# Kernel tuning notes

Measured on AMD Instinct MI355X. Metric: run time of the kernel, lower is better.

Reference implementation:

```python
import jax, jax.numpy as jnp
import numpy as np
import math

# ---- static configuration (matches init_kwargs) ----
METADATA = [64, 48, 32]   # channels per l = 0,1,2
MAX_L = 3                 # order_out
N_BATCH = 32768
fact = math.factorial

def _cg_complex(l1, m1, l2, m2, l3, m3):
    # Clebsch-Gordan coefficient <l1 m1 l2 m2 | l3 m3> via Racah formula
    if m1 + m2 != m3 or l3 < abs(l1 - l2) or l3 > l1 + l2:
        return 0.0
    pre = math.sqrt((2*l3+1) * fact(l1+l2-l3) * fact(l1-l2+l3) * fact(-l1+l2+l3) / fact(l1+l2+l3+1))
    pre *= math.sqrt(fact(l1+m1)*fact(l1-m1)*fact(l2+m2)*fact(l2-m2)*fact(l3+m3)*fact(l3-m3))
    kmin = max(0, l2-l3-m1, l1-l3+m2)
    kmax = min(l1+l2-l3, l1-m1, l2+m2)
    s = 0.0
    for k in range(kmin, kmax+1):
        s += (-1)**k / (fact(k)*fact(l1+l2-l3-k)*fact(l1-m1-k)*fact(l2+m2-k)*fact(l3-l2+m1+k)*fact(l3-l1-m2+k))
    return pre * s

def _U(l):
    # complex->real spherical harmonic change of basis, rows = real m', cols = complex m
    U = np.zeros((2*l+1, 2*l+1), dtype=np.complex128)
    for m in range(-l, l+1):
        r = m + l
        if m > 0:
            U[r, m+l] = (-1)**m / math.sqrt(2.0); U[r, -m+l] = 1.0/math.sqrt(2.0)
        elif m == 0:
            U[r, l] = 1.0
        else:
            U[r, m+l] = 1j/math.sqrt(2.0); U[r, -m+l] = -1j*(-1)**m/math.sqrt(2.0)
    return U

def _real_cg(l1, l2, l3):
    Cc = np.zeros((2*l1+1, 2*l2+1, 2*l3+1))
    for m1 in range(-l1, l1+1):
        for m2 in range(-l2, l2+1):
            for m3 in range(-l3, l3+1):
                Cc[m1+l1, m2+l2, m3+l3] = _cg_complex(l1, m1, l2, m2, l3, m3)
    T = np.einsum('am,bn,co,mno->abc', _U(l1), _U(l2), _U(l3).conj(), Cc.astype(np.complex128))
    T = T.imag if np.abs(T.imag).max() > np.abs(T.real).max() else T.real
    return np.ascontiguousarray(T).astype(np.float32)

# ---- static index structures ----
L_IN = len(METADATA)
OFF_IN = np.concatenate([[0], np.cumsum([METADATA[l]*(2*l+1) for l in range(L_IN)])]).astype(np.int64)
DIM_IN = int(OFF_IN[-1])  # 368
PATHS = []
for l1 in range(L_IN):
    for l2 in range(L_IN):
        for l3 in range(abs(l1-l2), min(l1+l2, MAX_L)+1):
            PATHS.append((l1, l2, l3, min(METADATA[l1], METADATA[l2])))
MD_OV = [0]*(MAX_L+1)
for (_, _, l3, ch) in PATHS:
    MD_OV[l3] = max(MD_OV[l3], ch)
OFF_OUT = np.concatenate([[0], np.cumsum([MD_OV[l]*(2*l+1) for l in range(MAX_L+1)])]).astype(np.int64)
DIM_OUT = int(OFF_OUT[-1])  # 672
CG = {(l1, l2, l3): jnp.asarray(_real_cg(l1, l2, l3)) for (l1, l2, l3, _) in PATHS}

_mix_id, _scat = [], []
_base = 0
for (l1, l2, l3, ch) in PATHS:
    for i in range(ch):
        for m in range(2*l3+1):
            _mix_id.append(_base + i)
            _scat.append(int(OFF_OUT[l3]) + i*(2*l3+1) + m)
    _base += ch
MIX_ID = jnp.asarray(np.array(_mix_id, dtype=np.int64))
SCATTER = jnp.asarray(np.array(_scat, dtype=np.int64))
N_MIX = _base  # 688

_chan_in = []
_cb = 0
for l in range(L_IN):
    for i in range(METADATA[l]):
        _chan_in += [_cb + i]*(2*l+1)
    _cb += METADATA[l]
CHAN_IN = jnp.asarray(np.array(_chan_in, dtype=np.int64))
N_KEEP = _cb  # 144
_kin, _kout = [], []
for l in range(L_IN):
    cp = min(METADATA[l], MD_OV[l])
    for i in range(cp):
        for m in range(2*l+1):
            _kin.append(int(OFF_IN[l]) + i*(2*l+1) + m)
            _kout.append(int(OFF_OUT[l]) + i*(2*l+1) + m)
KEEP_IN = jnp.asarray(np.array(_kin, dtype=np.int64))
KEEP_OUT = jnp.asarray(np.array(_kout, dtype=np.int64))

SQ3 = math.sqrt(3.0)

def setup_inputs() -> dict:
    key = jax.random.key(0)
    k1, k2, k3 = jax.random.split(key, 3)
    x = jax.random.normal(k1, (N_BATCH, DIM_IN), dtype=jnp.float32)
    keep_coeff = jax.random.uniform(k2, (N_KEEP,), minval=-SQ3, maxval=SQ3, dtype=jnp.float32)
    mix_coeff = jax.random.uniform(k3, (N_MIX,), minval=-SQ3, maxval=SQ3, dtype=jnp.float32)
    return {"x": x, "keep_coeff": keep_coeff, "mix_coeff": mix_coeff}

def reference(x, keep_coeff, mix_coeff):
    n = x.shape[0]
    # keep path: per-channel coeff broadcast over m components
    x_keep = x * keep_coeff[CHAN_IN]  # [N, 368]
    # CG tensor-product self-coupling (diagonal channel pairing per path)
    tps = []
    for (l1, l2, l3, ch) in PATHS:
        x1 = x[:, OFF_IN[l1]:OFF_IN[l1]+ch*(2*l1+1)].reshape(n, ch, 2*l1+1)
        x2 = x[:, OFF_IN[l2]:OFF_IN[l2]+ch*(2*l2+1)].reshape(n, ch, 2*l2+1)
        tps.append(jnp.einsum('nia,nib,abm->nim', x1, x2, CG[(l1, l2, l3)]).reshape(n, -1))
    cat = jnp.concatenate(tps, axis=1)  # [N, 2576] non-overlapped TP output
    cat = cat * 0.5 * mix_coeff[MIX_ID]
    # scatter (index_add) into overlapped output layout
    out = jnp.zeros((n, DIM_OUT), dtype=x.dtype).at[:, SCATTER].add(cat)
    # gather + add of keep path (index_select + add_)
    out = out.at[:, KEEP_OUT].add(x_keep[:, KEEP_IN])
    return out
```

## Files before the change

### kernel.cpp

```cpp
#include <hip/hip_runtime.h>


namespace cgc {

struct cplx { double re, im; };
constexpr cplx cmul(cplx a, cplx b){ return {a.re*b.re - a.im*b.im, a.re*b.im + a.im*b.re}; }

constexpr double cfact(int n){ double r = 1.0; for (int i = 2; i <= n; ++i) r *= i; return r; }
constexpr double cabsd(double x){ return x < 0 ? -x : x; }

constexpr double csqrtd(double x){
  if (x <= 0.0) return 0.0;
  double g = x > 1.0 ? x : 1.0;
  for (int i = 0; i < 48; ++i) g = 0.5*(g + x/g);
  return g;
}

constexpr double SQRT2 = csqrtd(2.0);

constexpr double cg_complex(int l1,int m1,int l2,int m2,int l3,int m3){
  if (m1 + m2 != m3) return 0.0;
  int lo = l1 > l2 ? l1 - l2 : l2 - l1;
  if (l3 < lo || l3 > l1 + l2) return 0.0;
  double pre = csqrtd((2*l3+1) * cfact(l1+l2-l3)*cfact(l1-l2+l3)*cfact(-l1+l2+l3)/cfact(l1+l2+l3+1));
  pre *= csqrtd(cfact(l1+m1)*cfact(l1-m1)*cfact(l2+m2)*cfact(l2-m2)*cfact(l3+m3)*cfact(l3-m3));
  int kmin = 0;
  if (l2-l3-m1 > kmin) kmin = l2-l3-m1;
  if (l1-l3+m2 > kmin) kmin = l1-l3+m2;
  int kmax = l1+l2-l3;
  if (l1-m1 < kmax) kmax = l1-m1;
  if (l2+m2 < kmax) kmax = l2+m2;
  double s = 0.0;
  for (int k = kmin; k <= kmax; ++k){
    double d = cfact(k)*cfact(l1+l2-l3-k)*cfact(l1-m1-k)*cfact(l2+m2-k)
             * cfact(l3-l2+m1+k)*cfact(l3-l1-m2+k);
    s += ((k & 1) ? -1.0 : 1.0) / d;
  }
  return pre * s;
}

constexpr cplx Uent(int l, int r, int c){
  int m = r - l;
  if (m > 0){
    if (c ==  m + l) return { ((m & 1) ? -1.0 : 1.0)/SQRT2, 0.0 };
    if (c == -m + l) return { 1.0/SQRT2, 0.0 };
    return {0.0, 0.0};
  } else if (m == 0){
    if (c == l) return {1.0, 0.0};
    return {0.0, 0.0};
  } else {
    int ma = -m;
    if (c ==  m + l) return { 0.0, 1.0/SQRT2 };
    if (c == -m + l) return { 0.0, -(((ma & 1) ? -1.0 : 1.0))/SQRT2 };
    return {0.0, 0.0};
  }
}

template<int L1,int L2,int L3>
struct CGData { float w[(2*L1+1)*(2*L2+1)*(2*L3+1)]; };

template<int L1,int L2,int L3>
constexpr CGData<L1,L2,L3> make_cg(){
  constexpr int D1 = 2*L1+1, D2 = 2*L2+1, D3 = 2*L3+1;
  cplx U1[D1*D1] = {}; cplx U2[D2*D2] = {}; cplx U3c[D3*D3] = {};
  for (int r = 0; r < D1; ++r) for (int c = 0; c < D1; ++c) U1[r*D1+c] = Uent(L1, r, c);
  for (int r = 0; r < D2; ++r) for (int c = 0; c < D2; ++c) U2[r*D2+c] = Uent(L2, r, c);
  for (int r = 0; r < D3; ++r) for (int c = 0; c < D3; ++c){
    cplx u = Uent(L3, r, c); u.im = -u.im; U3c[r*D3+c] = u;
  }
  double Cc[D1*D2*D3] = {};
  for (int m1 = -L1; m1 <= L1; ++m1)
    for (int m2 = -L2; m2 <= L2; ++m2){
      int m3 = m1 + m2;
      if (m3 < -L3 || m3 > L3) continue;
      Cc[((m1+L1)*D2 + (m2+L2))*D3 + (m3+L3)] = cg_complex(L1,m1,L2,m2,L3,m3);
    }
  double re[D1*D2*D3] = {}; double im[D1*D2*D3] = {};
  for (int a = 0; a < D1; ++a)
    for (int b = 0; b < D2; ++b)
      for (int c = 0; c < D3; ++c){
        double sre = 0.0, sim = 0.0;
        for (int m = 0; m < D1; ++m)
          for (int n = 0; n < D2; ++n){
            int o = m + n - L1 - L2 + L3;
            if (o < 0 || o >= D3) continue;
            double cc = Cc[(m*D2+n)*D3 + o];
            if (cc == 0.0) continue;
            cplx p = cmul(cmul(U1[a*D1+m], U2[b*D2+n]), U3c[c*D3+o]);
            sre += p.re * cc; sim += p.im * cc;
          }
        re[(a*D2+b)*D3+c] = sre; im[(a*D2+b)*D3+c] = sim;
      }
  double mre = 0.0, mim = 0.0;
  for (int k = 0; k < D1*D2*D3; ++k){
    if (cabsd(re[k]) > mre) mre = cabsd(re[k]);
    if (cabsd(im[k]) > mim) mim = cabsd(im[k]);
  }
  CGData<L1,L2,L3> outv{};
  for (int k = 0; k < D1*D2*D3; ++k){
    double v = (mim > mre) ? im[k] : re[k];
    outv.w[k] = (cabsd(v) < 1e-10) ? 0.0f : (float)v;
  }
  return outv;
}

}

template<int L1,int L2,int L3>
__device__ __forceinline__ void tp_path(const float* xa, const float* xb, float cmix, float* acc){
  constexpr cgc::CGData<L1,L2,L3> cg = cgc::make_cg<L1,L2,L3>();
  constexpr int D1 = 2*L1+1, D2 = 2*L2+1, D3 = 2*L3+1;
  float tmp[D3];
  #pragma unroll
  for (int m = 0; m < D3; ++m) tmp[m] = 0.0f;
  #pragma unroll
  for (int a = 0; a < D1; ++a){
    #pragma unroll
    for (int b = 0; b < D2; ++b){
      const float pr = xa[a] * xb[b];
      #pragma unroll
      for (int m = 0; m < D3; ++m){
        const float W = cg.w[(a*D2+b)*D3 + m];
        if (W != 0.0f) tmp[m] += W * pr;
      }
    }
  }
  #pragma unroll
  for (int m = 0; m < D3; ++m) acc[m] += cmix * tmp[m];
}


#define RPB 8

__global__ __launch_bounds__(256) void selfmix_kernel(
    const float* __restrict__ x, const float* __restrict__ keep,
    const float* __restrict__ mix, float* __restrict__ out, int n)
{
  __shared__ __align__(16) float xs[RPB * 368];
  __shared__ __align__(16) float os[RPB * 672];

  const int t = threadIdx.x;
  const long long blk  = blockIdx.x;
  const long long row0 = blk * RPB;

  {
    const long long nf4  = (long long)n * 92;
    const long long base = row0 * 92;
    const float4* __restrict__ x4 = (const float4*)x;
    float4* xs4 = (float4*)xs;
    if (base + t < nf4)                   xs4[t]       = x4[base + t];
    if (base + 256 + t < nf4)             xs4[256 + t] = x4[base + 256 + t];
    if (t < 224 && base + 512 + t < nf4)  xs4[512 + t] = x4[base + 512 + t];
  }
  __syncthreads();

  {
    const int rowL = t >> 5;
    const int i    = t & 31;
    if (row0 + rowL < n){
      const float* xr = xs + rowL * 368;
      float*     orw  = os + rowL * 672;
      float s = xr[i];
      float p[3], d[5];
      #pragma unroll
      for (int k = 0; k < 3; ++k) p[k] = xr[64 + i*3 + k];
      #pragma unroll
      for (int k = 0; k < 5; ++k) d[k] = xr[208 + i*5 + k];

      float o0 = 0.f;
      float o1[3] = {0.f,0.f,0.f};
      float o2[5] = {0.f,0.f,0.f,0.f,0.f};
      float o3[7] = {0.f,0.f,0.f,0.f,0.f,0.f,0.f};

      tp_path<0,0,0>(&s,&s, 0.5f*mix[  0+i], &o0);
      tp_path<0,1,1>(&s, p, 0.5f*mix[ 64+i],  o1);
      tp_path<0,2,2>(&s, d, 0.5f*mix[112+i],  o2);
      tp_path<1,0,1>( p,&s, 0.5f*mix[144+i],  o1);
      tp_path<1,1,0>( p, p, 0.5f*mix[192+i], &o0);
      tp_path<1,1,1>( p, p, 0.5f*mix[240+i],  o1);
      tp_path<1,1,2>( p, p, 0.5f*mix[288+i],  o2);
      tp_path<1,2,1>( p, d, 0.5f*mix[336+i],  o1);
      tp_path<1,2,2>( p, d, 0.5f*mix[368+i],  o2);
      tp_path<1,2,3>( p, d, 0.5f*mix[400+i],  o3);
      tp_path<2,0,2>( d,&s, 0.5f*mix[432+i],  o2);
      tp_path<2,1,1>( d, p, 0.5f*mix[464+i],  o1);
      tp_path<2,1,2>( d, p, 0.5f*mix[496+i],  o2);
      tp_path<2,1,3>( d, p, 0.5f*mix[528+i],  o3);
      tp_path<2,2,0>( d, d, 0.5f*mix[560+i], &o0);
      tp_path<2,2,1>( d, d, 0.5f*mix[592+i],  o1);
      tp_path<2,2,2>( d, d, 0.5f*mix[624+i],  o2);
      tp_path<2,2,3>( d, d, 0.5f*mix[656+i],  o3);

      o0 += keep[i] * s;
      const float k1 = keep[64+i], k2 = keep[112+i];
      #pragma unroll
      for (int k = 0; k < 3; ++k) o1[k] += k1 * p[k];
      #pragma unroll
      for (int k = 0; k < 5; ++k) o2[k] += k2 * d[k];

      orw[i] = o0;
      #pragma unroll
      for (int k = 0; k < 3; ++k) orw[ 64 + i*3 + k] = o1[k];
      #pragma unroll
      for (int k = 0; k < 5; ++k) orw[208 + i*5 + k] = o2[k];
      #pragma unroll
      for (int k = 0; k < 7; ++k) orw[448 + i*7 + k] = o3[k];
    }
  }

  if (t < 128){
    const int rowL = t >> 4;
    const int i    = 32 + (t & 15);
    if (row0 + rowL < n){
      const float* xr = xs + rowL * 368;
      float*     orw  = os + rowL * 672;
      float s = xr[i];
      float p[3];
      #pragma unroll
      for (int k = 0; k < 3; ++k) p[k] = xr[64 + i*3 + k];

      float o0 = 0.f;
      float o1[3] = {0.f,0.f,0.f};
      float o2[5] = {0.f,0.f,0.f,0.f,0.f};

      tp_path<0,0,0>(&s,&s, 0.5f*mix[  0+i], &o0);
      tp_path<0,1,1>(&s, p, 0.5f*mix[ 64+i],  o1);
      tp_path<1,0,1>( p,&s, 0.5f*mix[144+i],  o1);
      tp_path<1,1,0>( p, p, 0.5f*mix[192+i], &o0);
      tp_path<1,1,1>( p, p, 0.5f*mix[240+i],  o1);
      tp_path<1,1,2>( p, p, 0.5f*mix[288+i],  o2);

      o0 += keep[i] * s;
      const float k1 = keep[64+i];
      #pragma unroll
      for (int k = 0; k < 3; ++k) o1[k] += k1 * p[k];

      orw[i] = o0;
      #pragma unroll
      for (int k = 0; k < 3; ++k) orw[ 64 + i*3 + k] = o1[k];
      #pragma unroll
      for (int k = 0; k < 5; ++k) orw[208 + i*5 + k] = o2[k];
    }
  } else {
    const int t2   = t - 128;
    const int rowL = t2 >> 4;
    const int i    = 48 + (t2 & 15);
    if (row0 + rowL < n){
      const float s = xs[rowL*368 + i];
      float o0 = 0.f;
      tp_path<0,0,0>(&s,&s, 0.5f*mix[0+i], &o0);
      o0 += keep[i] * s;
      os[rowL*672 + i] = o0;
    }
  }
  __syncthreads();

  {
    const long long nf4o = (long long)n * 168;
    const long long base = row0 * 168;
    const float4* os4 = (const float4*)os;
    float4* __restrict__ o4 = (float4*)out;
    #pragma unroll
    for (int rnd = 0; rnd < 5; ++rnd){
      const int sidx = rnd*256 + t;
      if (base + sidx < nf4o) o4[base + sidx] = os4[sidx];
    }
    const int sidx = 5*256 + t;
    if (t < 64 && base + sidx < nf4o) o4[base + sidx] = os4[sidx];
  }
}

extern "C" void kernel_launch(void* const* d_in, const int* in_sizes, int n_in,
                              void* d_out, int out_size, void* d_ws, size_t ws_size,
                              hipStream_t stream)
{
  const float* x    = (const float*)d_in[0];
  const float* keep = (const float*)d_in[1];
  const float* mix  = (const float*)d_in[2];
  float* out = (float*)d_out;
  const int n = in_sizes[0] / 368;
  const int blocks = (n + RPB - 1) / RPB;
  selfmix_kernel<<<blocks, 256, 0, stream>>>(x, keep, mix, out, n);
}
```

Before: 131.6 us.

## Use persistent grid-stride blocks with register prefetch and wave-private rows

Replaces one block per 8 rows with a persistent grid of 1024 blocks that loop over row groups. Each iteration prefetches the next group's input into registers while computing the current one. Each wave owns two rows end to end, so the __syncthreads barriers are gone. The mix and keep coefficients are now loaded into registers once per thread instead of once per row group. This adds register pressure (launch bounds of 256 threads with 4 blocks per CU) and depends on wave-level ordering of shared memory accesses with no explicit barrier.

```diff
diff --git a/kernel.cpp b/kernel.cpp
--- a/kernel.cpp
+++ b/kernel.cpp
@@ -130,143 +130,186 @@
 }
 
 
-#define RPB 8
-
-__global__ __launch_bounds__(256) void selfmix_kernel(
+#define NBLK 1024
+
+__global__ __launch_bounds__(256, 4) void selfmix_kernel(
     const float* __restrict__ x, const float* __restrict__ keep,
     const float* __restrict__ mix, float* __restrict__ out, int n)
 {
-  __shared__ __align__(16) float xs[RPB * 368];
-  __shared__ __align__(16) float os[RPB * 672];
+  __shared__ __align__(16) float xs[8 * 368];
+  __shared__ __align__(16) float os[8 * 672];
 
   const int t = threadIdx.x;
-  const long long blk  = blockIdx.x;
-  const long long row0 = blk * RPB;
-
+  const int w = t >> 6;
+  const int l = t & 63;
+  const long long G = (n + 7) >> 3;
+
+  const float4* __restrict__ x4 = (const float4*)x;
+  float4* __restrict__ o4 = (float4*)out;
+  float4* xs4 = (float4*)xs;
+  const float4* os4 = (const float4*)os;
+  const long long nf4i = (long long)n * 92;
+  const long long nf4o = (long long)n * 168;
+
+  const int iA = l & 31;
+  float cmA[18];
   {
-    const long long nf4  = (long long)n * 92;
-    const long long base = row0 * 92;
-    const float4* __restrict__ x4 = (const float4*)x;
-    float4* xs4 = (float4*)xs;
-    if (base + t < nf4)                   xs4[t]       = x4[base + t];
-    if (base + 256 + t < nf4)             xs4[256 + t] = x4[base + 256 + t];
-    if (t < 224 && base + 512 + t < nf4)  xs4[512 + t] = x4[base + 512 + t];
-  }
-  __syncthreads();
-
-  {
-    const int rowL = t >> 5;
-    const int i    = t & 31;
-    if (row0 + rowL < n){
-      const float* xr = xs + rowL * 368;
-      float*     orw  = os + rowL * 672;
-      float s = xr[i];
-      float p[3], d[5];
+    const int MB[18] = {0,64,112,144,192,240,288,336,368,400,
+                        432,464,496,528,560,592,624,656};
+    #pragma unroll
+    for (int k = 0; k < 18; ++k) cmA[k] = 0.5f * mix[MB[k] + iA];
+  }
+  const float kA0 = keep[iA], kA1 = keep[64+iA], kA2 = keep[112+iA];
+
+  float cmB[6], kB0 = 0.f, kB1 = 0.f, cmC = 0.f, kC = 0.f;
+  int iB = 0, iC = 0;
+  if (l < 32){
+    iB = 32 + (l & 15);
+    const int MBb[6] = {0,64,144,192,240,288};
+    #pragma unroll
+    for (int k = 0; k < 6; ++k) cmB[k] = 0.5f * mix[MBb[k] + iB];
+    kB0 = keep[iB]; kB1 = keep[64+iB];
+  } else {
+    iC = 48 + (l & 15);
+    cmC = 0.5f * mix[iC]; kC = keep[iC];
+  }
+
+  const float4 F4Z = {0.f, 0.f, 0.f, 0.f};
+
+  long long g = blockIdx.x;
+  float4 n0 = F4Z, n1 = F4Z, n2 = F4Z;
+  if (g < G){
+    const long long b = g*736 + (long long)w*184;
+    if (b + l       < nf4i) n0 = x4[b + l];
+    if (b + 64 + l  < nf4i) n1 = x4[b + 64 + l];
+    if (l < 56 && b + 128 + l < nf4i) n2 = x4[b + 128 + l];
+  }
+
+  for (; g < G; g += NBLK){
+    const float4 c0 = n0, c1 = n1, c2 = n2;
+
+    const long long gn = g + NBLK;
+    if (gn < G){
+      const long long b = gn*736 + (long long)w*184;
+      if (b + l       < nf4i) n0 = x4[b + l];
+      if (b + 64 + l  < nf4i) n1 = x4[b + 64 + l];
+      if (l < 56 && b + 128 + l < nf4i) n2 = x4[b + 128 + l];
+    }
+
+    {
+      const int sb = w * 184;
+      xs4[sb + l] = c0;
+      xs4[sb + 64 + l] = c1;
+      if (l < 56) xs4[sb + 128 + l] = c2;
+    }
+
+    const long long row0 = g * 8;
+
+    {
+      const int rowL = w*2 + (l >> 5);
+      if (row0 + rowL < n){
+        const float* xr = xs + rowL * 368;
+        float*     orw  = os + rowL * 672;
+        const int i = iA;
+        float s = xr[i];
+        float p[3], d[5];
+        #pragma unroll
+        for (int k = 0; k < 3; ++k) p[k] = xr[64 + i*3 + k];
+        #pragma unroll
+        for (int k = 0; k < 5; ++k) d[k] = xr[208 + i*5 + k];
+
+        float o0 = 0.f;
+        float o1[3] = {0.f,0.f,0.f};
+        float o2[5] = {0.f,0.f,0.f,0.f,0.f};
+        float o3[7] = {0.f,0.f,0.f,0.f,0.f,0.f,0.f};
+
+        tp_path<0,0,0>(&s,&s, cmA[ 0], &o0);
+        tp_path<0,1,1>(&s, p, cmA[ 1],  o1);
+        tp_path<0,2,2>(&s, d, cmA[ 2],  o2);
+        tp_path<1,0,1>( p,&s, cmA[ 3],  o1);
+        tp_path<1,1,0>( p, p, cmA[ 4], &o0);
+        tp_path<1,1,1>( p, p, cmA[ 5],  o1);
+        tp_path<1,1,2>( p, p, cmA[ 6],  o2);
+        tp_path<1,2,1>( p, d, cmA[ 7],  o1);
+        tp_path<1,2,2>( p, d, cmA[ 8],  o2);
+        tp_path<1,2,3>( p, d, cmA[ 9],  o3);
+        tp_path<2,0,2>( d,&s, cmA[10],  o2);
+        tp_path<2,1,1>( d, p, cmA[11],  o1);
+        tp_path<2,1,2>( d, p, cmA[12],  o2);
+        tp_path<2,1,3>( d, p, cmA[13],  o3);
+        tp_path<2,2,0>( d, d, cmA[14], &o0);
+        tp_path<2,2,1>( d, d, cmA[15],  o1);
+        tp_path<2,2,2>( d, d, cmA[16],  o2);
+        tp_path<2,2,3>( d, d, cmA[17],  o3);
+
+        o0 += kA0 * s;
+        #pragma unroll
+        for (int k = 0; k < 3; ++k) o1[k] += kA1 * p[k];
+        #pragma unroll
+        for (int k = 0; k < 5; ++k) o2[k] += kA2 * d[k];
+
+        orw[i] = o0;
+        #pragma unroll
+        for (int k = 0; k < 3; ++k) orw[ 64 + i*3 + k] = o1[k];
+        #pragma unroll
+        for (int k = 0; k < 5; ++k) orw[208 + i*5 + k] = o2[k];
+        #pragma unroll
+        for (int k = 0; k < 7; ++k) orw[448 + i*7 + k] = o3[k];
+      }
+    }
+
+    if (l < 32){
+      const int rowL = w*2 + ((l >> 4) & 1);
+      if (row0 + rowL < n){
+        const float* xr = xs + rowL * 368;
+        float*     orw  = os + rowL * 672;
+        const int i = iB;
+        float s = xr[i];
+        float p[3];
+        #pragma unroll
+        for (int k = 0; k < 3; ++k) p[k] = xr[64 + i*3 + k];
+
+        float o0 = 0.f;
+        float o1[3] = {0.f,0.f,0.f};
+        float o2[5] = {0.f,0.f,0.f,0.f,0.f};
+
+        tp_path<0,0,0>(&s,&s, cmB[0], &o0);
+        tp_path<0,1,1>(&s, p, cmB[1],  o1);
+        tp_path<1,0,1>( p,&s, cmB[2],  o1);
+        tp_path<1,1,0>( p, p, cmB[3], &o0);
+        tp_path<1,1,1>( p, p, cmB[4],  o1);
+        tp_path<1,1,2>( p, p, cmB[5],  o2);
+
+        o0 += kB0 * s;
+        #pragma unroll
+        for (int k = 0; k < 3; ++k) o1[k] += kB1 * p[k];
+
+        orw[i] = o0;
+        #pragma unroll
+        for (int k = 0; k < 3; ++k) orw[ 64 + i*3 + k] = o1[k];
+        #pragma unroll
+        for (int k = 0; k < 5; ++k) orw[208 + i*5 + k] = o2[k];
+      }
+    } else {
+      const int rowL = w*2 + ((l >> 4) & 1);
+      if (row0 + rowL < n){
+        const float s = xs[rowL*368 + iC];
+        float o0 = 0.f;
+        tp_path<0,0,0>(&s,&s, cmC, &o0);
+        o0 += kC * s;
+        os[rowL*672 + iC] = o0;
+      }
+    }
+
+    {
+      const int sb = w * 336;
+      const long long ob = g*1344 + (long long)w*336;
       #pragma unroll
-      for (int k = 0; k < 3; ++k) p[k] = xr[64 + i*3 + k];
-      #pragma unroll
-      for (int k = 0; k < 5; ++k) d[k] = xr[208 + i*5 + k];
-
-      float o0 = 0.f;
-      float o1[3] = {0.f,0.f,0.f};
-      float o2[5] = {0.f,0.f,0.f,0.f,0.f};
-      float o3[7] = {0.f,0.f,0.f,0.f,0.f,0.f,0.f};
-
-      tp_path<0,0,0>(&s,&s, 0.5f*mix[  0+i], &o0);
-      tp_path<0,1,1>(&s, p, 0.5f*mix[ 64+i],  o1);
-      tp_path<0,2,2>(&s, d, 0.5f*mix[112+i],  o2);
-      tp_path<1,0,1>( p,&s, 0.5f*mix[144+i],  o1);
-      tp_path<1,1,0>( p, p, 0.5f*mix[192+i], &o0);
-      tp_path<1,1,1>( p, p, 0.5f*mix[240+i],  o1);
-      tp_path<1,1,2>( p, p, 0.5f*mix[288+i],  o2);
-      tp_path<1,2,1>( p, d, 0.5f*mix[336+i],  o1);
-      tp_path<1,2,2>( p, d, 0.5f*mix[368+i],  o2);
-      tp_path<1,2,3>( p, d, 0.5f*mix[400+i],  o3);
-      tp_path<2,0,2>( d,&s, 0.5f*mix[432+i],  o2);
-      tp_path<2,1,1>( d, p, 0.5f*mix[464+i],  o1);
-      tp_path<2,1,2>( d, p, 0.5f*mix[496+i],  o2);
-      tp_path<2,1,3>( d, p, 0.5f*mix[528+i],  o3);
-      tp_path<2,2,0>( d, d, 0.5f*mix[560+i], &o0);
-      tp_path<2,2,1>( d, d, 0.5f*mix[592+i],  o1);
-      tp_path<2,2,2>( d, d, 0.5f*mix[624+i],  o2);
-      tp_path<2,2,3>( d, d, 0.5f*mix[656+i],  o3);
-
-      o0 += keep[i] * s;
-      const float k1 = keep[64+i], k2 = keep[112+i];
-      #pragma unroll
-      for (int k = 0; k < 3; ++k) o1[k] += k1 * p[k];
-      #pragma unroll
-      for (int k = 0; k < 5; ++k) o2[k] += k2 * d[k];
-
-      orw[i] = o0;
-      #pragma unroll
-      for (int k = 0; k < 3; ++k) orw[ 64 + i*3 + k] = o1[k];
-      #pragma unroll
-      for (int k = 0; k < 5; ++k) orw[208 + i*5 + k] = o2[k];
-      #pragma unroll
-      for (int k = 0; k < 7; ++k) orw[448 + i*7 + k] = o3[k];
-    }
-  }
-
-  if (t < 128){
-    const int rowL = t >> 4;
-    const int i    = 32 + (t & 15);
-    if (row0 + rowL < n){
-      const float* xr = xs + rowL * 368;
-      float*     orw  = os + rowL * 672;
-      float s = xr[i];
-      float p[3];
-      #pragma unroll
-      for (int k = 0; k < 3; ++k) p[k] = xr[64 + i*3 + k];
-
-      float o0 = 0.f;
-      float o1[3] = {0.f,0.f,0.f};
-      float o2[5] = {0.f,0.f,0.f,0.f,0.f};
-
-      tp_path<0,0,0>(&s,&s, 0.5f*mix[  0+i], &o0);
-      tp_path<0,1,1>(&s, p, 0.5f*mix[ 64+i],  o1);
-      tp_path<1,0,1>( p,&s, 0.5f*mix[144+i],  o1);
-      tp_path<1,1,0>( p, p, 0.5f*mix[192+i], &o0);
-      tp_path<1,1,1>( p, p, 0.5f*mix[240+i],  o1);
-      tp_path<1,1,2>( p, p, 0.5f*mix[288+i],  o2);
-
-      o0 += keep[i] * s;
-      const float k1 = keep[64+i];
-      #pragma unroll
-      for (int k = 0; k < 3; ++k) o1[k] += k1 * p[k];
-
-      orw[i] = o0;
-      #pragma unroll
-      for (int k = 0; k < 3; ++k) orw[ 64 + i*3 + k] = o1[k];
-      #pragma unroll
-      for (int k = 0; k < 5; ++k) orw[208 + i*5 + k] = o2[k];
-    }
-  } else {
-    const int t2   = t - 128;
-    const int rowL = t2 >> 4;
-    const int i    = 48 + (t2 & 15);
-    if (row0 + rowL < n){
-      const float s = xs[rowL*368 + i];
-      float o0 = 0.f;
-      tp_path<0,0,0>(&s,&s, 0.5f*mix[0+i], &o0);
-      o0 += keep[i] * s;
-      os[rowL*672 + i] = o0;
-    }
-  }
-  __syncthreads();
-
-  {
-    const long long nf4o = (long long)n * 168;
-    const long long base = row0 * 168;
-    const float4* os4 = (const float4*)os;
-    float4* __restrict__ o4 = (float4*)out;
-    #pragma unroll
-    for (int rnd = 0; rnd < 5; ++rnd){
-      const int sidx = rnd*256 + t;
-      if (base + sidx < nf4o) o4[base + sidx] = os4[sidx];
-    }
-    const int sidx = 5*256 + t;
-    if (t < 64 && base + sidx < nf4o) o4[base + sidx] = os4[sidx];
+      for (int k = 0; k < 5; ++k){
+        if (ob + k*64 + l < nf4o) o4[ob + k*64 + l] = os4[sb + k*64 + l];
+      }
+      if (l < 16 && ob + 320 + l < nf4o) o4[ob + 320 + l] = os4[sb + 320 + l];
+    }
   }
 }
 
@@ -279,6 +322,7 @@
   const float* mix  = (const float*)d_in[2];
   float* out = (float*)d_out;
   const int n = in_sizes[0] / 368;
-  const int blocks = (n + RPB - 1) / RPB;
+  const long long G = (n + 7) >> 3;
+  const int blocks = (int)(G < NBLK ? G : NBLK);
   selfmix_kernel<<<blocks, 256, 0, stream>>>(x, keep, mix, out, n);
 }
```

Measured after the change: 185.0 us. 40.5% more time.
